# Kernel tuning notes

Hardware: AMD Instinct MI355X
Metric: run time of the kernel (lower is better)

Reference implementation:

```python
import jax, jax.numpy as jnp
import numpy as np

# near_sym_b (13,19)-tap biorthogonal level-1 DTCWT filters (Kingsbury)
H0O = np.array([-0.0017578125, 0.0, 0.022265625, -0.046875, -0.0482421875,
                0.296875, 0.5554687500, 0.296875, -0.0482421875, -0.046875,
                0.022265625, 0.0, -0.0017578125], dtype=np.float32)
H1O = np.array([-7.0626e-05, 0.0, 1.34189e-03, -1.88341e-03, -7.15660e-03,
                2.38560e-02, 5.56431e-02, -5.16881e-02, -2.99758e-01,
                5.59431e-01, -2.99758e-01, -5.16881e-02, 5.56431e-02,
                2.38560e-02, -7.15660e-03, -1.88341e-03, 1.34189e-03,
                0.0, -7.0626e-05], dtype=np.float32)

def _alt(h):
    c = (len(h) - 1) // 2
    return (h * ((-1.0) ** (np.arange(len(h)) - c))).astype(np.float32)

G0O = _alt(H1O)  # synthesis lowpass  (PR complement of H1O)
G1O = _alt(H0O)  # synthesis highpass (PR complement of H0O)

DIM, HS, WS, BATCH, NB, BS = 64, 56, 56, 32, 4, 16


def _filt(x, h, axis):
    # depthwise 1D correlation with symmetric padding; x: (B,C,H,W), axis in {2,3}
    L = len(h); p = L // 2
    pad = [(0, 0)] * 4; pad[axis] = (p, p)
    xp = jnp.pad(x, pad, mode='symmetric')
    k = jnp.asarray(h, x.dtype).reshape((1, 1, L, 1) if axis == 2 else (1, 1, 1, L))
    B, C = x.shape[:2]
    y = jax.lax.conv_general_dilated(
        xp.reshape((B * C, 1) + xp.shape[2:]), k, (1, 1), 'VALID',
        dimension_numbers=('NCHW', 'OIHW', 'NCHW'))
    return y.reshape((B, C) + y.shape[2:])


def _q2c(y):
    y = y * np.float32(1.0 / np.sqrt(2.0))
    a = y[..., 0::2, 0::2]; b = y[..., 0::2, 1::2]
    c = y[..., 1::2, 0::2]; d = y[..., 1::2, 1::2]
    return (a - d, b + c), (a + d, b - c)


def _c2q(w1r, w1i, w2r, w2i):
    sc = np.float32(1.0 / np.sqrt(2.0))
    B, C, Hh, Wh = w1r.shape
    top = jnp.stack([(w1r + w2r) * sc, (w1i + w2i) * sc], axis=-1).reshape(B, C, Hh, 2 * Wh)
    bot = jnp.stack([(w1i - w2i) * sc, (w2r - w1r) * sc], axis=-1).reshape(B, C, Hh, 2 * Wh)
    return jnp.stack([top, bot], axis=3).reshape(B, C, 2 * Hh, 2 * Wh)


def dtcwt_fwd_j1(x):
    lo = _filt(x, H0O, 3); hi = _filt(x, H1O, 3)
    ll = _filt(lo, H0O, 2)
    (d15r, d15i), (d165r, d165i) = _q2c(_filt(lo, H1O, 2))   # LH -> 15/165 deg
    (d75r, d75i), (d105r, d105i) = _q2c(_filt(hi, H0O, 2))   # HL -> 75/105 deg
    (d45r, d45i), (d135r, d135i) = _q2c(_filt(hi, H1O, 2))   # HH -> 45/135 deg
    real = jnp.stack([d15r, d45r, d75r, d105r, d135r, d165r], axis=2)
    imag = jnp.stack([d15i, d45i, d75i, d105i, d135i, d165i], axis=2)
    return ll, jnp.stack([real, imag], axis=-1)  # (B,C,H,W), (B,C,6,H/2,W/2,2)


def dtcwt_inv_j1(ll, yh):
    r = yh[..., 0]; im = yh[..., 1]
    lh = _c2q(r[:, :, 0], im[:, :, 0], r[:, :, 5], im[:, :, 5])
    hl = _c2q(r[:, :, 2], im[:, :, 2], r[:, :, 3], im[:, :, 3])
    hh = _c2q(r[:, :, 1], im[:, :, 1], r[:, :, 4], im[:, :, 4])
    lo = _filt(ll, G0O, 2) + _filt(lh, G1O, 2)
    hi = _filt(hl, G0O, 2) + _filt(hh, G1O, 2)
    return _filt(lo, G0O, 3) + _filt(hi, G1O, 3)


def setup_inputs():
    key = jax.random.key(0)
    ks = jax.random.split(key, 6)
    return {
        'x': jax.random.normal(ks[0], (BATCH, HS * WS, DIM), jnp.float32),
        'w_ll': jax.random.normal(ks[1], (DIM, HS, WS), jnp.float32) * 0.02,
        'w1': jax.random.normal(ks[2], (2, NB, BS, BS), jnp.float32) * 0.02,
        'w2': jax.random.normal(ks[3], (2, NB, BS, BS), jnp.float32) * 0.02,
        'b1': jax.random.normal(ks[4], (2, NB, BS), jnp.float32) * 0.02,
        'b2': jax.random.normal(ks[5], (2, NB, BS), jnp.float32) * 0.02,
        'H': HS, 'W': WS,
    }


def reference(x, w_ll, w1, w2, b1, b2, H, W):
    Bt, N, C = x.shape
    xi = jnp.transpose(x.reshape(Bt, H, W, C), (0, 3, 1, 2)).astype(jnp.float32)
    xl, xh = dtcwt_fwd_j1(xi)
    xl = xl * w_ll                                  # (B,C,H,W) * (C,H,W)
    Hh, Wh = H // 2, W // 2
    # (B,C,6,Hh,Wh,2) -> (2,B,6,Hh,Wh,C) -> split C into (NB,BS) blocks
    xh = jnp.transpose(xh, (5, 0, 2, 3, 4, 1)).reshape(2, Bt, 6, Hh, Wh, NB, BS)
    xr, xim = xh[0], xh[1]
    mul = lambda t, w: jnp.einsum('...bd,bdk->...bk', t, w)
    r1 = jax.nn.relu(mul(xr, w1[0]) - mul(xim, w1[1]) + b1[0])
    i1 = jax.nn.relu(mul(xr, w1[1]) + mul(xim, w1[0]) + b1[1])
    r2 = mul(r1, w2[0]) - mul(i1, w2[1]) + b2[0]
    i2 = mul(r1, w2[1]) + mul(i1, w2[0]) + b2[1]
    xh2 = jnp.stack([r2, i2], axis=-1).reshape(Bt, 6, Hh, Wh, C, 2)
    xh2 = jnp.transpose(xh2, (0, 4, 1, 2, 3, 5))    # (B,C,6,Hh,Wh,2)
    y = dtcwt_inv_j1(xl, xh2)
    return jnp.transpose(y, (0, 2, 3, 1)).reshape(Bt, N, C)
```

## Files before the change

### kernel.cpp

```cpp
#include <hip/hip_runtime.h>

#define BT 32
#define CH 64
#define HS 56
#define WS 56
#define HH 28
#define WH 28

namespace {
constexpr float ISQ2 = 0.70710678118654752440f;
constexpr float F_H0[13] = {-0.0017578125f, 0.0f, 0.022265625f, -0.046875f,
    -0.0482421875f, 0.296875f, 0.55546875f, 0.296875f, -0.0482421875f,
    -0.046875f, 0.022265625f, 0.0f, -0.0017578125f};
constexpr float F_H1[19] = {-7.0626e-05f, 0.0f, 0.00134189f, -0.00188341f,
    -0.0071566f, 0.023856f, 0.0556431f, -0.0516881f, -0.299758f, 0.559431f,
    -0.299758f, -0.0516881f, 0.0556431f, 0.023856f, -0.0071566f,
    -0.00188341f, 0.00134189f, 0.0f, -7.0626e-05f};
constexpr float F_G0[19] = {7.0626e-05f, 0.0f, -0.00134189f, -0.00188341f,
    0.0071566f, 0.023856f, -0.0556431f, -0.0516881f, 0.299758f, 0.559431f,
    0.299758f, -0.0516881f, -0.0556431f, 0.023856f, 0.0071566f,
    -0.00188341f, -0.00134189f, 0.0f, 7.0626e-05f};
constexpr float F_G1[13] = {-0.0017578125f, 0.0f, 0.022265625f, 0.046875f,
    -0.0482421875f, -0.296875f, 0.55546875f, -0.296875f, -0.0482421875f,
    0.046875f, 0.022265625f, 0.0f, -0.0017578125f};
}

__device__ __forceinline__ int symi(int k) {
    k = (k < 0) ? (-1 - k) : k;
    k = (k >= HS) ? (2 * HS - 1 - k) : k;
    return k;
}

__device__ __forceinline__ unsigned short f2bf(float f) {
    unsigned u = __float_as_uint(f);
    u += 0x7fffu + ((u >> 16) & 1u);
    return (unsigned short)(u >> 16);
}
__device__ __forceinline__ float bf2f(unsigned short h) {
    return __uint_as_float(((unsigned)h) << 16);
}
__device__ __forceinline__ float2 bfp2(unsigned u) {
    float2 r;
    r.x = __uint_as_float((u & 0xffffu) << 16);
    r.y = __uint_as_float(u & 0xffff0000u);
    return r;
}
__device__ __forceinline__ unsigned packbf(float a, float b) {
    return (unsigned)f2bf(a) | ((unsigned)f2bf(b) << 16);
}

typedef __attribute__((ext_vector_type(8))) short short8;
typedef __attribute__((ext_vector_type(4))) float f32x4;

#define PPOS 784

__global__ __launch_bounds__(256) void k_fwd_rows(const float* __restrict__ x,
                                                  unsigned short* __restrict__ lo,
                                                  unsigned short* __restrict__ hi,
                                                  const float* __restrict__ wll,
                                                  float* __restrict__ wllT) {
    int b = blockIdx.x / HS, h = blockIdx.x % HS;
    int strip = threadIdx.x >> 5;
    int c0 = (threadIdx.x & 31) * 2;
    int base = (b * HS + h) * WS * CH + c0;
    const float* row = x + base;
    unsigned short* lop = lo + base;
    unsigned short* hip = hi + base;
    int w0s = strip * 7;
    float Wa[19], Wb[19];
#pragma unroll
    for (int t = 0; t < 19; ++t) {
        float2 v = *(const float2*)(row + symi(w0s - 9 + t) * CH);
        Wa[t] = v.x; Wb[t] = v.y;
    }
    float2 nW[7];
#pragma unroll
    for (int u = 0; u < 7; ++u) nW[u] = *(const float2*)(row + symi(w0s + u + 10) * CH);
#pragma unroll
    for (int u = 0; u < 7; ++u) {
        int w = w0s + u;
        float aLo = 0.f, aHi = 0.f, bLo = 0.f, bHi = 0.f;
#pragma unroll
        for (int t = 0; t < 13; ++t) { aLo += F_H0[t] * Wa[3 + t]; bLo += F_H0[t] * Wb[3 + t]; }
#pragma unroll
        for (int t = 0; t < 19; ++t) { aHi += F_H1[t] * Wa[t]; bHi += F_H1[t] * Wb[t]; }
        *(unsigned*)(lop + w * CH) = packbf(aLo, bLo);
        *(unsigned*)(hip + w * CH) = packbf(aHi, bHi);
#pragma unroll
        for (int t = 0; t < 18; ++t) { Wa[t] = Wa[t + 1]; Wb[t] = Wb[t + 1]; }
        Wa[18] = nW[u].x; Wb[18] = nW[u].y;
    }
    if (blockIdx.x < 49) {
        __shared__ float tile[64][65];
        int pos0 = blockIdx.x * 64;
        int lp = threadIdx.x & 63, g = threadIdx.x >> 6;
#pragma unroll
        for (int r = 0; r < 16; ++r) {
            int cc = r * 4 + g;
            tile[cc][lp] = wll[cc * (HS * WS) + pos0 + lp];
        }
        __syncthreads();
#pragma unroll
        for (int r = 0; r < 16; ++r) {
            int pl = r * 4 + g;
            wllT[(pos0 + pl) * CH + lp] = tile[lp][pl];
        }
    }
}

__global__ __launch_bounds__(256) void k_cols(
    const unsigned short* __restrict__ lo_in,
    const unsigned short* __restrict__ hi_in, const float* __restrict__ wllT,
    float* __restrict__ xl, unsigned short* __restrict__ sbT) {
    __shared__ float qT[2][4][64][15];
    int hf = blockIdx.y;
    int zmode = blockIdx.z;
    int b = blockIdx.x / WH, wp = blockIdx.x % WH;
    int w0 = 2 * wp, tid = threadIdx.x;
    int q = tid >> 6, c = tid & 63;
    int rp = q >> 1, jc = q & 1;
    const unsigned short* srcp = zmode ? hi_in : lo_in;
    const unsigned short* colbase = srcp + (b * HS) * WS * CH + (w0 + jc) * CH + c;
    {
        int hstart = 2 * (hf * 14) + rp;
        float W[19];
#pragma unroll
        for (int t = 0; t < 19; ++t) W[t] = bf2f(colbase[symi(hstart - 9 + t) * (WS * CH)]);
        float nW0[14], nW1[14], nwll[14];
#pragma unroll
        for (int u = 0; u < 14; ++u) {
            int h = hstart + 2 * u;
            nW0[u] = bf2f(colbase[symi(h + 10) * (WS * CH)]);
            nW1[u] = bf2f(colbase[symi(h + 11) * (WS * CH)]);
        }
        if (zmode == 0) {
#pragma unroll
            for (int u = 0; u < 14; ++u)
                nwll[u] = wllT[((hstart + 2 * u) * WS + (w0 + jc)) * CH + c];
        }
#pragma unroll
        for (int u = 0; u < 14; ++u) {
            int h = hstart + 2 * u;
            float v0 = 0.f, v1 = 0.f;
#pragma unroll
            for (int t = 0; t < 13; ++t) v0 += F_H0[t] * W[3 + t];
#pragma unroll
            for (int t = 0; t < 19; ++t) v1 += F_H1[t] * W[t];
            if (zmode == 0) {
                xl[((b * HS + h) * WS + (w0 + jc)) * CH + c] = v0 * nwll[u];
                qT[0][q][c][u] = v1;
            } else {
                qT[0][q][c][u] = v0;
                qT[1][q][c][u] = v1;
            }
#pragma unroll
            for (int t = 0; t < 17; ++t) W[t] = W[t + 2];
            W[17] = nW0[u];
            W[18] = nW1[u];
        }
    }
    __syncthreads();
    {
        int qq = tid >> 5;
        int role = qq & 3, half = qq >> 2;
        int c0 = (tid & 31) * 2;
        int rowA = role & 1, rowB = 3 - (role & 1);
        float sgn = (role == 1 || role == 2) ? 1.f : -1.f;
        int posb = wp * 28 + hf * 14;
        if (zmode == 0) {
            int p = (role < 2) ? role : role + 8;
            const float* qA0 = &qT[0][rowA][c0][0];
            const float* qA1 = &qT[0][rowA][c0 + 1][0];
            const float* qB0 = &qT[0][rowB][c0][0];
            const float* qB1 = &qT[0][rowB][c0 + 1][0];
            unsigned short* dst = sbT + ((p * BT + b) * PPOS + posb) * CH + c0;
#pragma unroll
            for (int g = 0; g < 7; ++g) {
                int ii = half * 7 + g;
                float v0 = (qA0[ii] + sgn * qB0[ii]) * ISQ2;
                float v1 = (qA1[ii] + sgn * qB1[ii]) * ISQ2;
                *(unsigned*)(dst + ii * CH) = packbf(v0, v1);
            }
        } else {
#pragma unroll
            for (int src = 0; src < 2; ++src) {
                int p = (src == 0) ? (4 + role) : ((role < 2) ? (2 + role) : (6 + role));
                const float* qA0 = &qT[src][rowA][c0][0];
                const float* qA1 = &qT[src][rowA][c0 + 1][0];
                const float* qB0 = &qT[src][rowB][c0][0];
                const float* qB1 = &qT[src][rowB][c0 + 1][0];
                unsigned short* dst = sbT + ((p * BT + b) * PPOS + posb) * CH + c0;
#pragma unroll
                for (int g = 0; g < 7; ++g) {
                    int ii = half * 7 + g;
                    float v0 = (qA0[ii] + sgn * qB0[ii]) * ISQ2;
                    float v1 = (qA1[ii] + sgn * qB1[ii]) * ISQ2;
                    *(unsigned*)(dst + ii * CH) = packbf(v0, v1);
                }
            }
        }
    }
}

__global__ __launch_bounds__(256) void k_mix(
    const unsigned short* __restrict__ sbT, const float* __restrict__ w1,
    const float* __restrict__ w2, const float* __restrict__ b1,
    const float* __restrict__ b2, unsigned short* __restrict__ P0,
    unsigned short* __restrict__ P1, unsigned short* __restrict__ P2) {
    __shared__ unsigned short l1a[4][16][36];
    __shared__ unsigned short l1b[4][16][36];
    int blk = blockIdx.x;
    int pr = blk / (BT * 7);
    int rem = blk % (BT * 7);
    int b = rem / 7;
    int chunk = rem % 7;
    int sa = (pr == 0) ? 0 : (pr == 1) ? 2 : 1;
    int sb = (pr == 0) ? 5 : (pr == 1) ? 3 : 4;
    unsigned short* Pd = (pr == 0) ? P0 : (pr == 1) ? P1 : P2;
    int tid = threadIdx.x;
    int lane = tid & 63;
    int wv = tid >> 6;
    int nb = __builtin_amdgcn_readfirstlane(wv);
    int quad = lane >> 4;
    int n = lane & 15;

    short8 B1r, B1i, B2r, B2i;
#pragma unroll
    for (int j = 0; j < 8; ++j) {
        int kk = quad * 8 + j;
        int riw = kk >> 4, dd = kk & 15;
        float v1r = w1[nb * 256 + dd * 16 + n];
        float v1i = w1[1024 + nb * 256 + dd * 16 + n];
        float v2r = w2[nb * 256 + dd * 16 + n];
        float v2i = w2[1024 + nb * 256 + dd * 16 + n];
        B1r[j] = (short)f2bf(riw ? -v1i : v1r);
        B1i[j] = (short)f2bf(riw ? v1r : v1i);
        B2r[j] = (short)f2bf(riw ? -v2i : v2r);
        B2i[j] = (short)f2bf(riw ? v2r : v2i);
    }
    float bias1r = b1[nb * 16 + n], bias1i = b1[64 + nb * 16 + n];
    float bias2r = b2[nb * 16 + n], bias2i = b2[64 + nb * 16 + n];

    int rix = quad >> 1, dlo = (quad & 1) * 8;
    const unsigned short* pAa =
        sbT + (((sa * 2 + rix) * BT + b) * PPOS + n) * CH + nb * 16 + dlo;
    const unsigned short* pAb =
        sbT + (((sb * 2 + rix) * BT + b) * PPOS + n) * CH + nb * 16 + dlo;

    int pbase = chunk * 112;
    short8 A1a = *(const short8*)(pAa + pbase * CH);
    short8 A1b = *(const short8*)(pAb + pbase * CH);
    for (int t = 0; t < 7; ++t) {
        int pos0 = pbase + t * 16;
        short8 nAa = A1a, nAb = A1b;
        if (t < 6) {
            nAa = *(const short8*)(pAa + (pos0 + 16) * CH);
            nAb = *(const short8*)(pAb + (pos0 + 16) * CH);
        }
        f32x4 a1r = {bias1r, bias1r, bias1r, bias1r};
        f32x4 a1i = {bias1i, bias1i, bias1i, bias1i};
        f32x4 b1r_ = a1r, b1i_ = a1i;
        a1r = __builtin_amdgcn_mfma_f32_16x16x32_bf16(A1a, B1r, a1r, 0, 0, 0);
        a1i = __builtin_amdgcn_mfma_f32_16x16x32_bf16(A1a, B1i, a1i, 0, 0, 0);
        b1r_ = __builtin_amdgcn_mfma_f32_16x16x32_bf16(A1b, B1r, b1r_, 0, 0, 0);
        b1i_ = __builtin_amdgcn_mfma_f32_16x16x32_bf16(A1b, B1i, b1i_, 0, 0, 0);
#pragma unroll
        for (int r = 0; r < 4; ++r) {
            int pos = quad * 4 + r;
            l1a[wv][pos][n] = f2bf(fmaxf(a1r[r], 0.f));
            l1a[wv][pos][16 + n] = f2bf(fmaxf(a1i[r], 0.f));
            l1b[wv][pos][n] = f2bf(fmaxf(b1r_[r], 0.f));
            l1b[wv][pos][16 + n] = f2bf(fmaxf(b1i_[r], 0.f));
        }
        union { short8 s8; uint2 u2[2]; } a2a, a2b;
        const unsigned short* rowpa = &l1a[wv][n][0];
        const unsigned short* rowpb = &l1b[wv][n][0];
        a2a.u2[0] = *(const uint2*)(rowpa + quad * 8);
        a2a.u2[1] = *(const uint2*)(rowpa + quad * 8 + 4);
        a2b.u2[0] = *(const uint2*)(rowpb + quad * 8);
        a2b.u2[1] = *(const uint2*)(rowpb + quad * 8 + 4);
        f32x4 aAr = {bias2r, bias2r, bias2r, bias2r};
        f32x4 aAi = {bias2i, bias2i, bias2i, bias2i};
        f32x4 aBr = aAr, aBi = aAi;
        aAr = __builtin_amdgcn_mfma_f32_16x16x32_bf16(a2a.s8, B2r, aAr, 0, 0, 0);
        aAi = __builtin_amdgcn_mfma_f32_16x16x32_bf16(a2a.s8, B2i, aAi, 0, 0, 0);
        aBr = __builtin_amdgcn_mfma_f32_16x16x32_bf16(a2b.s8, B2r, aBr, 0, 0, 0);
        aBi = __builtin_amdgcn_mfma_f32_16x16x32_bf16(a2b.s8, B2i, aBi, 0, 0, 0);
#pragma unroll
        for (int r = 0; r < 4; ++r) {
            int pos_g = pos0 + quad * 4 + r;
            int wp = pos_g / 28, ii = pos_g - wp * 28;
            int o = ((b * HS + 2 * ii) * WS + 2 * wp) * CH + nb * 16 + n;
            Pd[o] = f2bf((aAr[r] + aBr[r]) * ISQ2);
            Pd[o + CH] = f2bf((aAi[r] + aBi[r]) * ISQ2);
            Pd[o + WS * CH] = f2bf((aAi[r] - aBi[r]) * ISQ2);
            Pd[o + WS * CH + CH] = f2bf((aBr[r] - aAr[r]) * ISQ2);
        }
        A1a = nAa; A1b = nAb;
    }
}

template <int MODE>
__device__ __forceinline__ void inv_cols_body(
    const float* __restrict__ xl, const unsigned short* __restrict__ P0,
    const unsigned short* __restrict__ P1, const unsigned short* __restrict__ P2,
    unsigned short* __restrict__ lo2, unsigned short* __restrict__ hi2) {
    int hf = blockIdx.y;
    int b = blockIdx.x / 7, wg = blockIdx.x % 7;
    int wl = threadIdx.x >> 5, l = threadIdx.x & 31;
    int c0 = l * 2;
    int w = wg * 8 + wl;
    int base = (b * HS) * WS * CH + w * CH + c0;
    const int st = WS * CH;
    const unsigned short* Bp = (MODE == 0) ? P0 : P2;
    unsigned short* outp = (MODE == 0) ? lo2 : hi2;
    auto ldA = [&](int r) -> float2 {
        if (MODE == 0) return *(const float2*)(xl + base + r * st);
        return bfp2(*(const unsigned*)(P1 + base + r * st));
    };
    auto ldB = [&](int r) -> float2 {
        return bfp2(*(const unsigned*)(Bp + base + r * st));
    };
    int h0 = hf * 28;
    float Aa[19], Ab[19], Ba[13], Bb[13];
#pragma unroll
    for (int t = 0; t < 19; ++t) { float2 v = ldA(symi(h0 - 9 + t)); Aa[t] = v.x; Ab[t] = v.y; }
#pragma unroll
    for (int t = 0; t < 13; ++t) { float2 v = ldB(symi(h0 - 6 + t)); Ba[t] = v.x; Bb[t] = v.y; }
    float2 pa0[4], pb0[4], pa1[4], pb1[4];
#define LDG(bA, bB, G)                                                          \
    {                                                                           \
        _Pragma("unroll") for (int u = 0; u < 4; ++u)                           \
            bA[u] = ldA(symi(h0 + (G) * 4 + u + 10));                           \
        _Pragma("unroll") for (int u = 0; u < 4; ++u)                           \
            bB[u] = ldB(symi(h0 + (G) * 4 + u + 7));                            \
    }
#define CPG(bA, bB, G)                                                          \
    {                                                                           \
        _Pragma("unroll") for (int u = 0; u < 4; ++u) {                         \
            int h = h0 + (G) * 4 + u;                                           \
            float acca = 0.f, accb = 0.f;                                       \
            _Pragma("unroll") for (int t = 0; t < 19; ++t) {                    \
                acca += F_G0[t] * Aa[t]; accb += F_G0[t] * Ab[t];               \
            }                                                                   \
            _Pragma("unroll") for (int t = 0; t < 13; ++t) {                    \
                acca += F_G1[t] * Ba[t]; accb += F_G1[t] * Bb[t];               \
            }                                                                   \
            *(unsigned*)(outp + base + h * st) = packbf(acca, accb);            \
            _Pragma("unroll") for (int t = 0; t < 18; ++t) {                    \
                Aa[t] = Aa[t + 1]; Ab[t] = Ab[t + 1];                           \
            }                                                                   \
            _Pragma("unroll") for (int t = 0; t < 12; ++t) {                    \
                Ba[t] = Ba[t + 1]; Bb[t] = Bb[t + 1];                           \
            }                                                                   \
            Aa[18] = bA[u].x; Ab[18] = bA[u].y;                                 \
            Ba[12] = bB[u].x; Bb[12] = bB[u].y;                                 \
        }                                                                       \
    }
    LDG(pa0, pb0, 0) LDG(pa1, pb1, 1)
    CPG(pa0, pb0, 0) LDG(pa0, pb0, 2)
    CPG(pa1, pb1, 1) LDG(pa1, pb1, 3)
    CPG(pa0, pb0, 2) LDG(pa0, pb0, 4)
    CPG(pa1, pb1, 3) LDG(pa1, pb1, 5)
    CPG(pa0, pb0, 4) LDG(pa0, pb0, 6)
    CPG(pa1, pb1, 5)
    CPG(pa0, pb0, 6)
#undef LDG
#undef CPG
}

__global__ __launch_bounds__(256) void k_inv_cols(
    const float* __restrict__ xl, const unsigned short* __restrict__ P0,
    const unsigned short* __restrict__ P1, const unsigned short* __restrict__ P2,
    unsigned short* __restrict__ lo2, unsigned short* __restrict__ hi2) {
    if (blockIdx.z == 0)
        inv_cols_body<0>(xl, P0, P1, P2, lo2, hi2);
    else
        inv_cols_body<1>(xl, P0, P1, P2, lo2, hi2);
}

__global__ __launch_bounds__(256) void k_inv_rows(
    const unsigned short* __restrict__ lo2,
    const unsigned short* __restrict__ hi2, float* __restrict__ out) {
    int b = blockIdx.x / HS, h = blockIdx.x % HS;
    int strip = threadIdx.x >> 5;
    int c0 = (threadIdx.x & 31) * 2;
    int base = (b * HS + h) * WS * CH + c0;
    const unsigned short* rlo = lo2 + base;
    const unsigned short* rhi = hi2 + base;
    float* op = out + base;
    int w0s = strip * 7;
    float Aa[19], Ab[19], Ba[13], Bb[13];
#pragma unroll
    for (int t = 0; t < 19; ++t) {
        float2 v = bfp2(*(const unsigned*)(rlo + symi(w0s - 9 + t) * CH));
        Aa[t] = v.x; Ab[t] = v.y;
    }
#pragma unroll
    for (int t = 0; t < 13; ++t) {
        float2 v = bfp2(*(const unsigned*)(rhi + symi(w0s - 6 + t) * CH));
        Ba[t] = v.x; Bb[t] = v.y;
    }
    float2 nA[7], nB[7];
#pragma unroll
    for (int u = 0; u < 7; ++u) nA[u] = bfp2(*(const unsigned*)(rlo + symi(w0s + u + 10) * CH));
#pragma unroll
    for (int u = 0; u < 7; ++u) nB[u] = bfp2(*(const unsigned*)(rhi + symi(w0s + u + 7) * CH));
#pragma unroll
    for (int u = 0; u < 7; ++u) {
        int w = w0s + u;
        float acca = 0.f, accb = 0.f;
#pragma unroll
        for (int t = 0; t < 19; ++t) { acca += F_G0[t] * Aa[t]; accb += F_G0[t] * Ab[t]; }
#pragma unroll
        for (int t = 0; t < 13; ++t) { acca += F_G1[t] * Ba[t]; accb += F_G1[t] * Bb[t]; }
        float2 ov; ov.x = acca; ov.y = accb;
        *(float2*)(op + w * CH) = ov;
#pragma unroll
        for (int t = 0; t < 18; ++t) { Aa[t] = Aa[t + 1]; Ab[t] = Ab[t + 1]; }
#pragma unroll
        for (int t = 0; t < 12; ++t) { Ba[t] = Ba[t + 1]; Bb[t] = Bb[t + 1]; }
        Aa[18] = nA[u].x; Ab[18] = nA[u].y;
        Ba[12] = nB[u].x; Bb[12] = nB[u].y;
    }
}

extern "C" void kernel_launch(void* const* d_in, const int* in_sizes, int n_in,
                              void* d_out, int out_size, void* d_ws, size_t ws_size,
                              hipStream_t stream) {
    const float* x = (const float*)d_in[0];
    const float* w_ll = (const float*)d_in[1];
    const float* w1 = (const float*)d_in[2];
    const float* w2 = (const float*)d_in[3];
    const float* b1 = (const float*)d_in[4];
    const float* b2 = (const float*)d_in[5];
    float* out = (float*)d_out;

    const size_t A = (size_t)BT * HS * WS * CH;
    const size_t SBf = (size_t)12 * 64 * BT * PPOS / 2;
    float* wsf = (float*)d_ws;
    float* xl = wsf;
    unsigned short* sbT = (unsigned short*)(wsf + A);
    unsigned short* lo2 = (unsigned short*)(wsf + A);
    unsigned short* hi2 = (unsigned short*)(wsf + A + SBf);
    unsigned short* lo_in = (unsigned short*)(wsf + A + SBf + A);
    unsigned short* hi_in = lo_in + A;
    unsigned short* P0 = hi_in + A;
    unsigned short* P1 = P0 + A;
    unsigned short* P2 = P1 + A;

    float* wllT = out;

    k_fwd_rows<<<BT * HS, 256, 0, stream>>>(x, lo_in, hi_in, w_ll, wllT);
    k_cols<<<dim3(BT * WH, 2, 2), 256, 0, stream>>>(lo_in, hi_in, wllT, xl, sbT);
    k_mix<<<3 * BT * 7, 256, 0, stream>>>(sbT, w1, w2, b1, b2, P0, P1, P2);
    k_inv_cols<<<dim3(BT * 7, 2, 2), 256, 0, stream>>>(xl, P0, P1, P2, lo2, hi2);
    k_inv_rows<<<BT * HS, 256, 0, stream>>>(lo2, hi2, out);
}
```

Baseline: 173.0 us.

## Store lowpass band as bf16 and split mixing kernel into one-tile blocks

The lowpass intermediate xl is now written by the column pass as bf16 instead of fp32, which halves its write and read traffic between the forward-column and inverse-column kernels. The mixing kernel no longer loops over seven 16-position tiles per block with software prefetch. It now launches seven times more blocks, each handling a single tile, to raise parallelism and occupancy. The cost is reduced precision on the lowpass path and redundant weight/bias loads and bf16 conversion in every small block.

```diff
diff --git a/kernel.cpp b/kernel.cpp
--- a/kernel.cpp
+++ b/kernel.cpp
@@ -111,7 +111,7 @@
 __global__ __launch_bounds__(256) void k_cols(
     const unsigned short* __restrict__ lo_in,
     const unsigned short* __restrict__ hi_in, const float* __restrict__ wllT,
-    float* __restrict__ xl, unsigned short* __restrict__ sbT) {
+    unsigned short* __restrict__ xl, unsigned short* __restrict__ sbT) {
     __shared__ float qT[2][4][64][15];
     int hf = blockIdx.y;
     int zmode = blockIdx.z;
@@ -147,7 +147,7 @@
 #pragma unroll
             for (int t = 0; t < 19; ++t) v1 += F_H1[t] * W[t];
             if (zmode == 0) {
-                xl[((b * HS + h) * WS + (w0 + jc)) * CH + c] = v0 * nwll[u];
+                xl[((b * HS + h) * WS + (w0 + jc)) * CH + c] = f2bf(v0 * nwll[u]);
                 qT[0][q][c][u] = v1;
             } else {
                 qT[0][q][c][u] = v0;
@@ -210,10 +210,10 @@
     __shared__ unsigned short l1a[4][16][36];
     __shared__ unsigned short l1b[4][16][36];
     int blk = blockIdx.x;
-    int pr = blk / (BT * 7);
-    int rem = blk % (BT * 7);
-    int b = rem / 7;
-    int chunk = rem % 7;
+    int pr = blk / (BT * 49);
+    int rem = blk % (BT * 49);
+    int b = rem / 49;
+    int tile = rem % 49;
     int sa = (pr == 0) ? 0 : (pr == 1) ? 2 : 1;
     int sb = (pr == 0) ? 5 : (pr == 1) ? 3 : 4;
     unsigned short* Pd = (pr == 0) ? P0 : (pr == 1) ? P1 : P2;
@@ -223,6 +223,15 @@
     int nb = __builtin_amdgcn_readfirstlane(wv);
     int quad = lane >> 4;
     int n = lane & 15;
+
+    int rix = quad >> 1, dlo = (quad & 1) * 8;
+    int pos0 = tile * 16;
+    const unsigned short* pAa =
+        sbT + (((sa * 2 + rix) * BT + b) * PPOS + pos0 + n) * CH + nb * 16 + dlo;
+    const unsigned short* pAb =
+        sbT + (((sb * 2 + rix) * BT + b) * PPOS + pos0 + n) * CH + nb * 16 + dlo;
+    short8 A1a = *(const short8*)pAa;
+    short8 A1b = *(const short8*)pAb;
 
     short8 B1r, B1i, B2r, B2i;
 #pragma unroll
@@ -241,68 +250,50 @@
     float bias1r = b1[nb * 16 + n], bias1i = b1[64 + nb * 16 + n];
     float bias2r = b2[nb * 16 + n], bias2i = b2[64 + nb * 16 + n];
 
-    int rix = quad >> 1, dlo = (quad & 1) * 8;
-    const unsigned short* pAa =
-        sbT + (((sa * 2 + rix) * BT + b) * PPOS + n) * CH + nb * 16 + dlo;
-    const unsigned short* pAb =
-        sbT + (((sb * 2 + rix) * BT + b) * PPOS + n) * CH + nb * 16 + dlo;
-
-    int pbase = chunk * 112;
-    short8 A1a = *(const short8*)(pAa + pbase * CH);
-    short8 A1b = *(const short8*)(pAb + pbase * CH);
-    for (int t = 0; t < 7; ++t) {
-        int pos0 = pbase + t * 16;
-        short8 nAa = A1a, nAb = A1b;
-        if (t < 6) {
-            nAa = *(const short8*)(pAa + (pos0 + 16) * CH);
-            nAb = *(const short8*)(pAb + (pos0 + 16) * CH);
-        }
-        f32x4 a1r = {bias1r, bias1r, bias1r, bias1r};
-        f32x4 a1i = {bias1i, bias1i, bias1i, bias1i};
-        f32x4 b1r_ = a1r, b1i_ = a1i;
-        a1r = __builtin_amdgcn_mfma_f32_16x16x32_bf16(A1a, B1r, a1r, 0, 0, 0);
-        a1i = __builtin_amdgcn_mfma_f32_16x16x32_bf16(A1a, B1i, a1i, 0, 0, 0);
-        b1r_ = __builtin_amdgcn_mfma_f32_16x16x32_bf16(A1b, B1r, b1r_, 0, 0, 0);
-        b1i_ = __builtin_amdgcn_mfma_f32_16x16x32_bf16(A1b, B1i, b1i_, 0, 0, 0);
-#pragma unroll
-        for (int r = 0; r < 4; ++r) {
-            int pos = quad * 4 + r;
-            l1a[wv][pos][n] = f2bf(fmaxf(a1r[r], 0.f));
-            l1a[wv][pos][16 + n] = f2bf(fmaxf(a1i[r], 0.f));
-            l1b[wv][pos][n] = f2bf(fmaxf(b1r_[r], 0.f));
-            l1b[wv][pos][16 + n] = f2bf(fmaxf(b1i_[r], 0.f));
-        }
-        union { short8 s8; uint2 u2[2]; } a2a, a2b;
-        const unsigned short* rowpa = &l1a[wv][n][0];
-        const unsigned short* rowpb = &l1b[wv][n][0];
-        a2a.u2[0] = *(const uint2*)(rowpa + quad * 8);
-        a2a.u2[1] = *(const uint2*)(rowpa + quad * 8 + 4);
-        a2b.u2[0] = *(const uint2*)(rowpb + quad * 8);
-        a2b.u2[1] = *(const uint2*)(rowpb + quad * 8 + 4);
-        f32x4 aAr = {bias2r, bias2r, bias2r, bias2r};
-        f32x4 aAi = {bias2i, bias2i, bias2i, bias2i};
-        f32x4 aBr = aAr, aBi = aAi;
-        aAr = __builtin_amdgcn_mfma_f32_16x16x32_bf16(a2a.s8, B2r, aAr, 0, 0, 0);
-        aAi = __builtin_amdgcn_mfma_f32_16x16x32_bf16(a2a.s8, B2i, aAi, 0, 0, 0);
-        aBr = __builtin_amdgcn_mfma_f32_16x16x32_bf16(a2b.s8, B2r, aBr, 0, 0, 0);
-        aBi = __builtin_amdgcn_mfma_f32_16x16x32_bf16(a2b.s8, B2i, aBi, 0, 0, 0);
-#pragma unroll
-        for (int r = 0; r < 4; ++r) {
-            int pos_g = pos0 + quad * 4 + r;
-            int wp = pos_g / 28, ii = pos_g - wp * 28;
-            int o = ((b * HS + 2 * ii) * WS + 2 * wp) * CH + nb * 16 + n;
-            Pd[o] = f2bf((aAr[r] + aBr[r]) * ISQ2);
-            Pd[o + CH] = f2bf((aAi[r] + aBi[r]) * ISQ2);
-            Pd[o + WS * CH] = f2bf((aAi[r] - aBi[r]) * ISQ2);
-            Pd[o + WS * CH + CH] = f2bf((aBr[r] - aAr[r]) * ISQ2);
-        }
-        A1a = nAa; A1b = nAb;
+    f32x4 a1r = {bias1r, bias1r, bias1r, bias1r};
+    f32x4 a1i = {bias1i, bias1i, bias1i, bias1i};
+    f32x4 b1r_ = a1r, b1i_ = a1i;
+    a1r = __builtin_amdgcn_mfma_f32_16x16x32_bf16(A1a, B1r, a1r, 0, 0, 0);
+    a1i = __builtin_amdgcn_mfma_f32_16x16x32_bf16(A1a, B1i, a1i, 0, 0, 0);
+    b1r_ = __builtin_amdgcn_mfma_f32_16x16x32_bf16(A1b, B1r, b1r_, 0, 0, 0);
+    b1i_ = __builtin_amdgcn_mfma_f32_16x16x32_bf16(A1b, B1i, b1i_, 0, 0, 0);
+#pragma unroll
+    for (int r = 0; r < 4; ++r) {
+        int pos = quad * 4 + r;
+        l1a[wv][pos][n] = f2bf(fmaxf(a1r[r], 0.f));
+        l1a[wv][pos][16 + n] = f2bf(fmaxf(a1i[r], 0.f));
+        l1b[wv][pos][n] = f2bf(fmaxf(b1r_[r], 0.f));
+        l1b[wv][pos][16 + n] = f2bf(fmaxf(b1i_[r], 0.f));
+    }
+    union { short8 s8; uint2 u2[2]; } a2a, a2b;
+    const unsigned short* rowpa = &l1a[wv][n][0];
+    const unsigned short* rowpb = &l1b[wv][n][0];
+    a2a.u2[0] = *(const uint2*)(rowpa + quad * 8);
+    a2a.u2[1] = *(const uint2*)(rowpa + quad * 8 + 4);
+    a2b.u2[0] = *(const uint2*)(rowpb + quad * 8);
+    a2b.u2[1] = *(const uint2*)(rowpb + quad * 8 + 4);
+    f32x4 aAr = {bias2r, bias2r, bias2r, bias2r};
+    f32x4 aAi = {bias2i, bias2i, bias2i, bias2i};
+    f32x4 aBr = aAr, aBi = aAi;
+    aAr = __builtin_amdgcn_mfma_f32_16x16x32_bf16(a2a.s8, B2r, aAr, 0, 0, 0);
+    aAi = __builtin_amdgcn_mfma_f32_16x16x32_bf16(a2a.s8, B2i, aAi, 0, 0, 0);
+    aBr = __builtin_amdgcn_mfma_f32_16x16x32_bf16(a2b.s8, B2r, aBr, 0, 0, 0);
+    aBi = __builtin_amdgcn_mfma_f32_16x16x32_bf16(a2b.s8, B2i, aBi, 0, 0, 0);
+#pragma unroll
+    for (int r = 0; r < 4; ++r) {
+        int pos_g = pos0 + quad * 4 + r;
+        int wp = pos_g / 28, ii = pos_g - wp * 28;
+        int o = ((b * HS + 2 * ii) * WS + 2 * wp) * CH + nb * 16 + n;
+        Pd[o] = f2bf((aAr[r] + aBr[r]) * ISQ2);
+        Pd[o + CH] = f2bf((aAi[r] + aBi[r]) * ISQ2);
+        Pd[o + WS * CH] = f2bf((aAi[r] - aBi[r]) * ISQ2);
+        Pd[o + WS * CH + CH] = f2bf((aBr[r] - aAr[r]) * ISQ2);
     }
 }
 
 template <int MODE>
 __device__ __forceinline__ void inv_cols_body(
-    const float* __restrict__ xl, const unsigned short* __restrict__ P0,
+    const unsigned short* __restrict__ xl, const unsigned short* __restrict__ P0,
     const unsigned short* __restrict__ P1, const unsigned short* __restrict__ P2,
     unsigned short* __restrict__ lo2, unsigned short* __restrict__ hi2) {
     int hf = blockIdx.y;
@@ -312,11 +303,11 @@
     int w = wg * 8 + wl;
     int base = (b * HS) * WS * CH + w * CH + c0;
     const int st = WS * CH;
+    const unsigned short* Ap = (MODE == 0) ? xl : P1;
     const unsigned short* Bp = (MODE == 0) ? P0 : P2;
     unsigned short* outp = (MODE == 0) ? lo2 : hi2;
     auto ldA = [&](int r) -> float2 {
-        if (MODE == 0) return *(const float2*)(xl + base + r * st);
-        return bfp2(*(const unsigned*)(P1 + base + r * st));
+        return bfp2(*(const unsigned*)(Ap + base + r * st));
     };
     auto ldB = [&](int r) -> float2 {
         return bfp2(*(const unsigned*)(Bp + base + r * st));
@@ -370,7 +361,7 @@
 }
 
 __global__ __launch_bounds__(256) void k_inv_cols(
-    const float* __restrict__ xl, const unsigned short* __restrict__ P0,
+    const unsigned short* __restrict__ xl, const unsigned short* __restrict__ P0,
     const unsigned short* __restrict__ P1, const unsigned short* __restrict__ P2,
     unsigned short* __restrict__ lo2, unsigned short* __restrict__ hi2) {
     if (blockIdx.z == 0)
@@ -439,7 +430,7 @@
     const size_t A = (size_t)BT * HS * WS * CH;
     const size_t SBf = (size_t)12 * 64 * BT * PPOS / 2;
     float* wsf = (float*)d_ws;
-    float* xl = wsf;
+    unsigned short* xl = (unsigned short*)wsf;
     unsigned short* sbT = (unsigned short*)(wsf + A);
     unsigned short* lo2 = (unsigned short*)(wsf + A);
     unsigned short* hi2 = (unsigned short*)(wsf + A + SBf);
@@ -453,7 +444,7 @@
 
     k_fwd_rows<<<BT * HS, 256, 0, stream>>>(x, lo_in, hi_in, w_ll, wllT);
     k_cols<<<dim3(BT * WH, 2, 2), 256, 0, stream>>>(lo_in, hi_in, wllT, xl, sbT);
-    k_mix<<<3 * BT * 7, 256, 0, stream>>>(sbT, w1, w2, b1, b2, P0, P1, P2);
+    k_mix<<<3 * BT * 49, 256, 0, stream>>>(sbT, w1, w2, b1, b2, P0, P1, P2);
     k_inv_cols<<<dim3(BT * 7, 2, 2), 256, 0, stream>>>(xl, P0, P1, P2, lo2, hi2);
     k_inv_rows<<<BT * HS, 256, 0, stream>>>(lo2, hi2, out);
 }
```

New measurement: 165.2 us. 4.5% less time.
